# Optimization experiments

Hardware: AMD Instinct MI355X
Metric: run time of the kernel (lower is better)

The kernel has to match this reference:

```python
import jax, jax.numpy as jnp
import numpy as np

V = 4096      # num codes (vocab)
D = 128       # embedding dim
K = 3         # diffusion scales
H = 4         # attn heads
FF = 128      # ff hidden
L = 2         # attn layers
NVIS = 8192   # visits
MAXC = 32     # max codes per visit
PAD = 0


def logmap0(x):
    # Poincare ball (c=1) log map at origin: artanh(||x||) * x / ||x||
    eps = 1e-7
    norm = jnp.linalg.norm(x, axis=-1, keepdims=True)
    norm_c = jnp.clip(norm, eps, 1.0 - 1e-5)
    return jnp.arctanh(norm_c) * x / jnp.maximum(norm, eps)


def layer_norm(x, g, b, eps=1e-5):
    m = jnp.mean(x, axis=-1, keepdims=True)
    v = jnp.mean((x - m) ** 2, axis=-1, keepdims=True)
    return (x - m) * jax.lax.rsqrt(v + eps) * g + b


def attn_block(x, Wqkv, bqkv, Wo, bo, W1, b1, W2, b2, g1, be1, g2, be2):
    # x: [V, D] (batch of 1, squeezed)
    hd = D // H
    qkv = x @ Wqkv.T + bqkv                      # [V, 3D]
    q, k, v = jnp.split(qkv, 3, axis=-1)
    q = q.reshape(V, H, hd)
    k = k.reshape(V, H, hd)
    v = v.reshape(V, H, hd)
    scores = jnp.einsum('shd,thd->hst', q, k) / np.sqrt(hd).astype(x.dtype)
    a = jax.nn.softmax(scores, axis=-1)          # [H, V, V]
    o = jnp.einsum('hst,thd->shd', a, v).reshape(V, D)
    attn_out = o @ Wo.T + bo
    x = layer_norm(x + attn_out, g1, be1)
    ff = jax.nn.gelu(x @ W1.T + b1) @ W2.T + b2
    return layer_norm(x + ff, g2, be2)


def setup_inputs() -> dict:
    key = jax.random.key(0)
    ks = jax.random.split(key, 20)
    inp = {}
    inp['visits'] = jax.random.randint(ks[0], (NVIS, MAXC), 0, V)
    # hyperbolic points inside unit ball
    inp['X_hyp'] = jax.random.normal(ks[1], (V, D), jnp.float32) * 0.01
    inp['kernels'] = jax.random.normal(ks[2], (K, V, V), jnp.float32) / V
    inp['proj_W'] = jax.random.normal(ks[3], (D, K * D), jnp.float32) * 0.05
    inp['proj_b'] = jnp.zeros((D,), jnp.float32)
    s = 0.05
    inp['Wqkv'] = jax.random.normal(ks[4], (L, 3 * D, D), jnp.float32) * s
    inp['bqkv'] = jnp.zeros((L, 3 * D), jnp.float32)
    inp['Wo'] = jax.random.normal(ks[5], (L, D, D), jnp.float32) * s
    inp['bo'] = jnp.zeros((L, D), jnp.float32)
    inp['W1'] = jax.random.normal(ks[6], (L, FF, D), jnp.float32) * s
    inp['b1'] = jnp.zeros((L, FF), jnp.float32)
    inp['W2'] = jax.random.normal(ks[7], (L, D, FF), jnp.float32) * s
    inp['b2'] = jnp.zeros((L, D), jnp.float32)
    inp['ln1_g'] = jnp.ones((L, D), jnp.float32)
    inp['ln1_b'] = jnp.zeros((L, D), jnp.float32)
    inp['ln2_g'] = jnp.ones((L, D), jnp.float32)
    inp['ln2_b'] = jnp.zeros((L, D), jnp.float32)
    return inp


def reference(visits, X_hyp, kernels, proj_W, proj_b, Wqkv, bqkv, Wo, bo,
              W1, b1, W2, b2, ln1_g, ln1_b, ln2_g, ln2_b):
    # ---- hyperbolic graph diffusion ----
    Z0 = logmap0(X_hyp)                              # [V, D]
    Z_scales = jnp.einsum('kuv,vd->ukd', kernels, Z0)  # [V, K, D]
    Z_cat = Z_scales.reshape(V, K * D)
    H_ = Z_cat @ proj_W.T + proj_b                   # [V, D]
    # ---- global self-attention stack ----
    for l in range(L):
        H_ = attn_block(H_, Wqkv[l], bqkv[l], Wo[l], bo[l],
                        W1[l], b1[l], W2[l], b2[l],
                        ln1_g[l], ln1_b[l], ln2_g[l], ln2_b[l])
    # ---- per-visit masked mean pooling (segment mean) ----
    mask = (visits != PAD)                           # [NVIS, MAXC]
    gathered = H_[visits] * mask[..., None]          # [NVIS, MAXC, D]
    cnt = jnp.sum(mask, axis=-1, keepdims=True).astype(H_.dtype)
    summed = jnp.sum(gathered, axis=1)               # [NVIS, D]
    return jnp.where(cnt > 0, summed / jnp.maximum(cnt, 1.0), 0.0)
```

## Files before the change

### kernel.cpp

```cpp
#include <hip/hip_runtime.h>
#include <hip/hip_bf16.h>
#include <math.h>

#define VN 4096
#define DIM 128
#define KS 3
#define NH 4
#define HD 32
#define NVIS 8192
#define MAXC 32
#define KTOT (KS*VN)

typedef unsigned short u16;
typedef __attribute__((ext_vector_type(8))) short short8;
typedef __attribute__((ext_vector_type(4))) float f32x4;
typedef __attribute__((ext_vector_type(4))) float f4v;

__device__ __forceinline__ u16 f2b(float f){
  union { float f; unsigned u; } c; c.f = f;
  unsigned u = c.u;
  return (u16)((u + 0x7fffu + ((u >> 16) & 1u)) >> 16);
}
__device__ __forceinline__ float b2f(u16 x){
  union { float f; unsigned u; } c; c.u = ((unsigned)x) << 16; return c.f;
}
__device__ __forceinline__ unsigned cvt2(float lo, float hi){
  unsigned r;
  asm("v_cvt_pk_bf16_f32 %0, %1, %2" : "=v"(r) : "v"(lo), "v"(hi));
  return r;
}
#define MFMA16(a,b,c) __builtin_amdgcn_mfma_f32_16x16x32_bf16((a),(b),(c),0,0,0)

__global__ __launch_bounds__(256) void k_logmap(const float* __restrict__ xh, u16* __restrict__ z0){
  __shared__ float xs[64][132];
  __shared__ float part[4][64];
  __shared__ float sscale[64];
  int t = threadIdx.x;
  int v0 = blockIdx.x * 64;
  #pragma unroll
  for(int i=0;i<8;i++){
    int id = t + 256*i; int e = id*4; int r = e>>7; int c = e&127;
    float4 u = *(const float4*)&xh[(size_t)(v0+r)*DIM + c];
    xs[r][c+0]=u.x; xs[r][c+1]=u.y; xs[r][c+2]=u.z; xs[r][c+3]=u.w;
  }
  __syncthreads();
  int r = t & 63, q = t >> 6;
  float p = 0.f;
  #pragma unroll
  for(int c=0;c<32;c++){ float x = xs[r][q*32+c]; p += x*x; }
  part[q][r] = p;
  __syncthreads();
  if(t < 64){
    float ss = part[0][t]+part[1][t]+part[2][t]+part[3][t];
    float n = sqrtf(ss);
    float nc = fminf(fmaxf(n, 1e-7f), 1.0f - 1e-5f);
    sscale[t] = atanhf(nc) / fmaxf(n, 1e-7f);
  }
  __syncthreads();
  #pragma unroll
  for(int i=0;i<8;i++){
    int id = t + 256*i; int e = id*4; int rr = e>>7; int cc = e&127;
    float s = sscale[rr];
    uint2 o = { cvt2(xs[rr][cc+0]*s, xs[rr][cc+1]*s),
                cvt2(xs[rr][cc+2]*s, xs[rr][cc+3]*s) };
    *(uint2*)&z0[(size_t)(v0+rr)*DIM + cc] = o;
  }
}

template<bool AF32, bool BF32>
__device__ __forceinline__ void gemm_k128_t(const void* __restrict__ Agv, int lda,
                                            const void* __restrict__ Bgv, int ldb,
                                            u16 (*As)[128*72], u16 (*Bs)[128*72], f32x4 (&acc)[2][8]){
  int t = threadIdx.x;
  int w=t>>6, lane=t&63, l15=lane&15, quad=lane>>4;
  #pragma unroll
  for(int s=0;s<2;s++)
    #pragma unroll
    for(int n=0;n<8;n++) acc[s][n] = (f32x4){0.f,0.f,0.f,0.f};

  float4 af[4][2]; uint4 ai[4];
  float4 bf[4][2]; uint4 bi[4];

  auto LOAD = [&](int kb){
    #pragma unroll
    for(int i=0;i<4;i++){
      int id = t + 256*i; int row = id>>3, c8 = id&7;
      if constexpr(AF32){
        const float* Ag = (const float*)Agv;
        af[i][0] = *(const float4*)&Ag[(size_t)row*lda + kb + c8*8];
        af[i][1] = *(const float4*)&Ag[(size_t)row*lda + kb + c8*8 + 4];
      } else {
        const u16* Ag = (const u16*)Agv;
        ai[i] = *(const uint4*)&Ag[(size_t)row*lda + kb + c8*8];
      }
      if constexpr(BF32){
        const float* Bg = (const float*)Bgv;
        bf[i][0] = *(const float4*)&Bg[(size_t)row*ldb + kb + c8*8];
        bf[i][1] = *(const float4*)&Bg[(size_t)row*ldb + kb + c8*8 + 4];
      } else {
        const u16* Bg = (const u16*)Bgv;
        bi[i] = *(const uint4*)&Bg[(size_t)row*ldb + kb + c8*8];
      }
    }
  };
  auto COMMIT = [&](u16* Ad, u16* Bd){
    #pragma unroll
    for(int i=0;i<4;i++){
      int id = t + 256*i; int row = id>>3, c8 = id&7;
      if constexpr(AF32){
        uint4 p = { cvt2(af[i][0].x, af[i][0].y), cvt2(af[i][0].z, af[i][0].w),
                    cvt2(af[i][1].x, af[i][1].y), cvt2(af[i][1].z, af[i][1].w) };
        *(uint4*)&Ad[row*72 + c8*8] = p;
      } else {
        *(uint4*)&Ad[row*72 + c8*8] = ai[i];
      }
      if constexpr(BF32){
        uint4 q = { cvt2(bf[i][0].x, bf[i][0].y), cvt2(bf[i][0].z, bf[i][0].w),
                    cvt2(bf[i][1].x, bf[i][1].y), cvt2(bf[i][1].z, bf[i][1].w) };
        *(uint4*)&Bd[row*72 + c8*8] = q;
      } else {
        *(uint4*)&Bd[row*72 + c8*8] = bi[i];
      }
    }
  };
  auto COMPUTE = [&](const u16* Asb, const u16* Bsb){
    #pragma unroll
    for(int ks=0; ks<2; ks++){
      short8 a[2], b[8];
      #pragma unroll
      for(int s=0;s<2;s++) a[s] = *(const short8*)&Asb[(w*32+s*16+l15)*72 + (ks*4+quad)*8];
      #pragma unroll
      for(int n=0;n<8;n++)  b[n] = *(const short8*)&Bsb[(n*16+l15)*72 + (ks*4+quad)*8];
      #pragma unroll
      for(int s=0;s<2;s++)
        #pragma unroll
        for(int n=0;n<8;n++) acc[s][n] = MFMA16(a[s], b[n], acc[s][n]);
    }
  };

  LOAD(0);  COMMIT(As[0], Bs[0]);  __syncthreads();
  LOAD(64); COMPUTE(As[0], Bs[0]); COMMIT(As[1], Bs[1]); __syncthreads();
  COMPUTE(As[1], Bs[1]);
}

__global__ __launch_bounds__(256) void k_gproj(const float* __restrict__ projW, const u16* __restrict__ z0,
                                               u16* __restrict__ gbuf){
  __shared__ u16 As[2][128*72], Bs[2][128*72];
  int kb = blockIdx.x >> 5, vt = blockIdx.x & 31;
  f32x4 acc[2][8];
  gemm_k128_t<true,false>(projW + kb*128, 3*DIM, z0 + (size_t)vt*128*DIM, DIM, As, Bs, acc);
  int t=threadIdx.x, w=t>>6, lane=t&63, l15=lane&15, quad=lane>>4;
  #pragma unroll
  for(int s=0;s<2;s++)
    #pragma unroll
    for(int n=0;n<8;n++)
      #pragma unroll
      for(int rg=0;rg<4;rg++){
        int d = w*32 + s*16 + quad*4 + rg;
        int v = vt*128 + n*16 + l15;
        gbuf[(size_t)(d*KS + kb)*VN + v] = f2b(acc[s][n][rg]);
      }
}

__global__ __launch_bounds__(256) void k_diff(const float* __restrict__ kers, const u16* __restrict__ gbuf,
                                              u16* __restrict__ hpart){
  __shared__ u16 As[2][128*72], Bs[2][128*72];
  int t = threadIdx.x;
  int mt = blockIdx.x & 31;
  int sl = blockIdx.x >> 5;
  int w=t>>6, lane=t&63, l15=lane&15, quad=lane>>4;
  f32x4 acc[2][8];
  #pragma unroll
  for(int s=0;s<2;s++)
    #pragma unroll
    for(int n=0;n<8;n++) acc[s][n] = (f32x4){0.f,0.f,0.f,0.f};
  int k0 = sl * 768;

  f4v  fa0[4], fa1[4];
  uint4 fb[4];

  auto LOADSTEP = [&](int step){
    int kk = k0 + step*64;
    int kout = kk >> 12; int vv = kk & 4095;
    #pragma unroll
    for(int i=0;i<4;i++){
      int id = t + 256*i; int row = id>>3, c8 = id&7;
      const float* ap = &kers[((size_t)kout<<24) + (size_t)(mt*128+row)*VN + vv + c8*8];
      fa0[i] = __builtin_nontemporal_load((const f4v*)ap);
      fa1[i] = __builtin_nontemporal_load((const f4v*)(ap+4));
      fb[i]  = *(const uint4*)&gbuf[(size_t)row*KTOT + kk + c8*8];
    }
  };
  auto COMMIT = [&](u16* Ad, u16* Bd){
    #pragma unroll
    for(int i=0;i<4;i++){
      int id = t + 256*i; int row = id>>3, c8 = id&7;
      uint4 pa = { cvt2(fa0[i].x, fa0[i].y), cvt2(fa0[i].z, fa0[i].w),
                   cvt2(fa1[i].x, fa1[i].y), cvt2(fa1[i].z, fa1[i].w) };
      *(uint4*)&Ad[row*72 + c8*8] = pa;
      *(uint4*)&Bd[row*72 + c8*8] = fb[i];
    }
  };
  auto COMPUTE = [&](const u16* Asb, const u16* Bsb){
    #pragma unroll
    for(int ks=0; ks<2; ks++){
      short8 a[2], b[8];
      #pragma unroll
      for(int s=0;s<2;s++) a[s] = *(const short8*)&Asb[(w*32+s*16+l15)*72 + (ks*4+quad)*8];
      #pragma unroll
      for(int n=0;n<8;n++)  b[n] = *(const short8*)&Bsb[(n*16+l15)*72 + (ks*4+quad)*8];
      #pragma unroll
      for(int s=0;s<2;s++)
        #pragma unroll
        for(int n=0;n<8;n++) acc[s][n] = MFMA16(a[s], b[n], acc[s][n]);
    }
  };

  LOADSTEP(0);
  COMMIT(As[0], Bs[0]);
  __syncthreads();
  #pragma unroll 1
  for(int sp=0; sp<6; sp++){
    LOADSTEP(2*sp+1);
    COMPUTE(As[0], Bs[0]);
    COMMIT(As[1], Bs[1]);
    __syncthreads();
    if(sp < 5){
      LOADSTEP(2*sp+2);
      COMPUTE(As[1], Bs[1]);
      COMMIT(As[0], Bs[0]);
      __syncthreads();
    }
  }
  COMPUTE(As[1], Bs[1]);

  u16* dst = hpart + ((size_t)blockIdx.x << 14);
  #pragma unroll
  for(int s=0;s<2;s++)
    #pragma unroll
    for(int n=0;n<8;n++)
      #pragma unroll
      for(int rg=0;rg<4;rg++)
        dst[(w*32+s*16+quad*4+rg)*128 + n*16 + l15] = f2b(acc[s][n][rg]);
}

__global__ __launch_bounds__(256) void k_hreduce(const u16* __restrict__ hpart, const float* __restrict__ pb,
                                                 float* __restrict__ h0){
  int idx = blockIdx.x*256 + threadIdx.x;
  int e0 = idx*4;
  int c0 = e0 & 127;
  float4 r;
  r.x = pb[c0+0]; r.y = pb[c0+1]; r.z = pb[c0+2]; r.w = pb[c0+3];
  #pragma unroll
  for(int sl=0; sl<16; sl++){
    uint2 u = *(const uint2*)&hpart[((size_t)sl<<19) + e0];
    r.x += b2f((u16)(u.x & 0xffffu)); r.y += b2f((u16)(u.x >> 16));
    r.z += b2f((u16)(u.y & 0xffffu)); r.w += b2f((u16)(u.y >> 16));
  }
  *(float4*)&h0[e0] = r;
}

template<bool AF32>
__global__ __launch_bounds__(256) void k_qkv(const void* __restrict__ xb, const float* __restrict__ Wq,
                                             const float* __restrict__ bq, u16* __restrict__ outq){
  __shared__ u16 As[2][128*72], Bs[2][128*72];
  int mt = blockIdx.x & 31, ntile = blockIdx.x >> 5;
  f32x4 acc[2][8];
  const void* Ap = AF32 ? (const void*)((const float*)xb + (size_t)mt*128*DIM)
                        : (const void*)((const u16*)xb + (size_t)mt*128*DIM);
  gemm_k128_t<AF32,true>(Ap, DIM, Wq + (size_t)ntile*128*DIM, DIM, As, Bs, acc);
  int t=threadIdx.x, w=t>>6, lane=t&63, l15=lane&15, quad=lane>>4;
  #pragma unroll
  for(int s=0;s<2;s++)
    #pragma unroll
    for(int n=0;n<8;n++)
      #pragma unroll
      for(int rg=0;rg<4;rg++){
        int row = mt*128 + w*32 + s*16 + quad*4 + rg;
        int col = ntile*128 + n*16 + l15;
        outq[(size_t)row*(3*DIM) + col] = f2b(acc[s][n][rg] + bq[col]);
      }
}

__global__ __launch_bounds__(256) void k_attn(const u16* __restrict__ qkv, float* __restrict__ opart,
                                              float* __restrict__ mlpart){
  __shared__ u16 Qs[64*40];
  __shared__ u16 Ksh[2][128*40];
  __shared__ u16 Vt[2][32*136];
  __shared__ u16 Ps[4*16*136];
  int t=threadIdx.x;
  int b = blockIdx.x;
  int h = b>>7, qt = (b>>1)&63, half = b&1;
  int w=t>>6, lane=t&63, l15=lane&15, quad=lane>>4;
  { int r = t>>2, c = t&3;
    *(uint4*)&Qs[r*40 + c*8] = *(const uint4*)&qkv[(size_t)(qt*64+r)*(3*DIM) + h*HD + c*8];
  }
  int skey = t>>2, sc4 = t&3;
  uint4 kreg[2], vreg[2];
  #pragma unroll
  for(int i=0;i<2;i++){
    int key = skey + 64*i;
    kreg[i] = *(const uint4*)&qkv[(size_t)((size_t)(half*16)*128+key)*(3*DIM) + DIM + h*HD + sc4*8];
    vreg[i] = *(const uint4*)&qkv[(size_t)((size_t)(half*16)*128+key)*(3*DIM) + 2*DIM + h*HD + sc4*8];
  }
  #pragma unroll
  for(int i=0;i<2;i++){
    int key = skey + 64*i;
    *(uint4*)&Ksh[0][key*40 + sc4*8] = kreg[i];
    u16 tmp[8]; *(uint4*)tmp = vreg[i];
    #pragma unroll
    for(int j=0;j<8;j++) Vt[0][(sc4*8+j)*136 + key] = tmp[j];
  }
  __syncthreads();
  short8 aq = *(short8*)&Qs[(w*16+l15)*40 + quad*8];
  f32x4 oacc[2]; oacc[0]=(f32x4){0.f,0.f,0.f,0.f}; oacc[1]=(f32x4){0.f,0.f,0.f,0.f};
  float mrun[4], lrun[4];
  #pragma unroll
  for(int rg=0;rg<4;rg++){ mrun[rg] = -INFINITY; lrun[rg] = 0.f; }
  const float sc = 0.17677669529663687f;
  for(int kti=0;kti<16;kti++){
    int cur = kti&1;
    if(kti<15){
      int kt = half*16 + kti + 1;
      #pragma unroll
      for(int i=0;i<2;i++){
        int key = skey + 64*i;
        kreg[i] = *(const uint4*)&qkv[(size_t)(kt*128+key)*(3*DIM) + DIM + h*HD + sc4*8];
        vreg[i] = *(const uint4*)&qkv[(size_t)(kt*128+key)*(3*DIM) + 2*DIM + h*HD + sc4*8];
      }
    }
    f32x4 s[8];
    #pragma unroll
    for(int n=0;n<8;n++)
      s[n] = MFMA16(aq, *(short8*)&Ksh[cur][(n*16+l15)*40 + quad*8], ((f32x4){0.f,0.f,0.f,0.f}));
    float mx[4];
    #pragma unroll
    for(int rg=0;rg<4;rg++){
      float m = -INFINITY;
      #pragma unroll
      for(int n=0;n<8;n++) m = fmaxf(m, s[n][rg]);
      #pragma unroll
      for(int off=1;off<16;off<<=1) m = fmaxf(m, __shfl_xor(m, off, 64));
      mx[rg] = m;
    }
    float alpha[4], rs[4];
    #pragma unroll
    for(int rg=0;rg<4;rg++){
      float mn = fmaxf(mrun[rg], mx[rg]);
      alpha[rg] = __expf(sc*(mrun[rg] - mn));
      mrun[rg] = mn; rs[rg] = 0.f;
    }
    #pragma unroll
    for(int n=0;n<8;n++)
      #pragma unroll
      for(int rg=0;rg<4;rg++){
        float p = __expf(sc*(s[n][rg] - mrun[rg]));
        s[n][rg] = p; rs[rg] += p;
      }
    #pragma unroll
    for(int rg=0;rg<4;rg++){
      #pragma unroll
      for(int off=1;off<16;off<<=1) rs[rg] += __shfl_xor(rs[rg], off, 64);
      lrun[rg] = lrun[rg]*alpha[rg] + rs[rg];
      oacc[0][rg] *= alpha[rg]; oacc[1][rg] *= alpha[rg];
    }
    #pragma unroll
    for(int n=0;n<8;n++)
      #pragma unroll
      for(int rg=0;rg<4;rg++)
        Ps[w*16*136 + (quad*4+rg)*136 + n*16 + l15] = f2b(s[n][rg]);
    #pragma unroll
    for(int kt2=0;kt2<4;kt2++){
      short8 ap = *(short8*)&Ps[w*16*136 + l15*136 + kt2*32 + quad*8];
      #pragma unroll
      for(int n2=0;n2<2;n2++)
        oacc[n2] = MFMA16(ap, *(short8*)&Vt[cur][(n2*16+l15)*136 + kt2*32 + quad*8], oacc[n2]);
    }
    if(kti<15){
      #pragma unroll
      for(int i=0;i<2;i++){
        int key = skey + 64*i;
        *(uint4*)&Ksh[cur^1][key*40 + sc4*8] = kreg[i];
        u16 tmp[8]; *(uint4*)tmp = vreg[i];
        #pragma unroll
        for(int j=0;j<8;j++) Vt[cur^1][(sc4*8+j)*136 + key] = tmp[j];
      }
    }
    __syncthreads();
  }
  float* op = opart + ((size_t)b << 11);
  #pragma unroll
  for(int n2=0;n2<2;n2++)
    #pragma unroll
    for(int rg=0;rg<4;rg++)
      op[(w*16+quad*4+rg)*32 + n2*16 + l15] = oacc[n2][rg];
  if(l15 == 0){
    float* ml = mlpart + ((size_t)b << 7);
    #pragma unroll
    for(int rg=0;rg<4;rg++){
      int r = w*16 + quad*4 + rg;
      ml[r] = sc*mrun[rg]; ml[64 + r] = lrun[rg];
    }
  }
}

__global__ __launch_bounds__(256) void k_oprojln(const float* __restrict__ opart, const float* __restrict__ mlpart,
                                                 const float* __restrict__ W,
                                                 const float* __restrict__ bias, const float* __restrict__ resf,
                                                 const float* __restrict__ g, const float* __restrict__ bb,
                                                 float* __restrict__ outf, u16* __restrict__ outb){
  __shared__ u16 As[128*72], Bs[128*72];
  int mt = blockIdx.x;
  int t=threadIdx.x, w=t>>6, lane=t&63, l15=lane&15, quad=lane>>4;
  f32x4 acc[2][8];
  #pragma unroll
  for(int s=0;s<2;s++)
    #pragma unroll
    for(int n=0;n<8;n++) acc[s][n] = (f32x4){0.f,0.f,0.f,0.f};
  #pragma unroll
  for(int step=0; step<2; step++){
    int kb = step*64;
    __syncthreads();
    #pragma unroll
    for(int i=0;i<4;i++){
      int id = t + 256*i; int row = id>>3, c8 = id&7;
      int col = kb + c8*8;
      int hh = col>>5, c0 = col&31;
      int grow = mt*128 + row;
      int hq = hh*64 + (grow>>6);
      int rr = grow & 63;
      const float* o0  = opart  + ((size_t)(hq*2)   << 11);
      const float* o1  = opart  + ((size_t)(hq*2+1) << 11);
      const float* ml0 = mlpart + ((size_t)(hq*2)   << 7);
      const float* ml1 = mlpart + ((size_t)(hq*2+1) << 7);
      float m0 = ml0[rr], l0 = ml0[64+rr], m1 = ml1[rr], l1 = ml1[64+rr];
      float m = fmaxf(m0, m1);
      float w0 = __expf(m0 - m), w1 = __expf(m1 - m);
      float inv = 1.f / (l0*w0 + l1*w1);
      float4 a0 = *(const float4*)&o0[rr*32 + c0];
      float4 a1 = *(const float4*)&o0[rr*32 + c0 + 4];
      float4 c0v = *(const float4*)&o1[rr*32 + c0];
      float4 c1v = *(const float4*)&o1[rr*32 + c0 + 4];
      uint4 pa = { cvt2((a0.x*w0+c0v.x*w1)*inv, (a0.y*w0+c0v.y*w1)*inv),
                   cvt2((a0.z*w0+c0v.z*w1)*inv, (a0.w*w0+c0v.w*w1)*inv),
                   cvt2((a1.x*w0+c1v.x*w1)*inv, (a1.y*w0+c1v.y*w1)*inv),
                   cvt2((a1.w*0.f + a1.x*w0 + c1v.x*w1)*inv*0.f + (a1.w*w0+c1v.w*w1)*inv, (a1.w*w0+c1v.w*w1)*inv) };
      pa.w = cvt2((a1.z*w0+c1v.z*w1)*inv, (a1.w*w0+c1v.w*w1)*inv);
      *(uint4*)&As[row*72 + c8*8] = pa;
      float4 f0 = *(const float4*)&W[(size_t)row*DIM + kb + c8*8];
      float4 f1 = *(const float4*)&W[(size_t)row*DIM + kb + c8*8 + 4];
      uint4 qa = { cvt2(f0.x, f0.y), cvt2(f0.z, f0.w),
                   cvt2(f1.x, f1.y), cvt2(f1.z, f1.w) };
      *(uint4*)&Bs[row*72 + c8*8] = qa;
    }
    __syncthreads();
    #pragma unroll
    for(int ks=0; ks<2; ks++){
      short8 a[2], b[8];
      #pragma unroll
      for(int s=0;s<2;s++) a[s] = *(short8*)&As[(w*32+s*16+l15)*72 + (ks*4+quad)*8];
      #pragma unroll
      for(int n=0;n<8;n++)  b[n] = *(short8*)&Bs[(n*16+l15)*72 + (ks*4+quad)*8];
      #pragma unroll
      for(int s=0;s<2;s++)
        #pragma unroll
        for(int n=0;n<8;n++) acc[s][n] = MFMA16(a[s], b[n], acc[s][n]);
    }
  }
  #pragma unroll
  for(int s=0;s<2;s++)
    #pragma unroll
    for(int n=0;n<8;n++)
      #pragma unroll
      for(int rg=0;rg<4;rg++){
        int row = mt*128 + w*32 + s*16 + quad*4 + rg;
        int col = n*16 + l15;
        acc[s][n][rg] += bias[col] + resf[(size_t)row*DIM + col];
      }
  #pragma unroll
  for(int s=0;s<2;s++)
    #pragma unroll
    for(int rg=0;rg<4;rg++){
      float a=0.f, bsum=0.f;
      #pragma unroll
      for(int n=0;n<8;n++){ float x = acc[s][n][rg]; a += x; bsum += x*x; }
      #pragma unroll
      for(int off=1;off<16;off<<=1){ a += __shfl_xor(a, off, 64); bsum += __shfl_xor(bsum, off, 64); }
      float mean = a*(1.f/128.f);
      float var  = bsum*(1.f/128.f) - mean*mean;
      float rstd = rsqrtf(var + 1e-5f);
      #pragma unroll
      for(int n=0;n<8;n++){
        int row = mt*128 + w*32 + s*16 + quad*4 + rg;
        int col = n*16 + l15;
        float y = (acc[s][n][rg] - mean)*rstd*g[col] + bb[col];
        outf[(size_t)row*DIM + col] = y;
        outb[(size_t)row*DIM + col] = f2b(y);
      }
    }
}

__global__ __launch_bounds__(256) void k_projln(const u16* __restrict__ Ab, const float* __restrict__ W,
                                                const float* __restrict__ bias, const float* __restrict__ resf,
                                                const float* __restrict__ g, const float* __restrict__ bb,
                                                float* __restrict__ outf, u16* __restrict__ outb){
  __shared__ u16 As[2][128*72], Bs[2][128*72];
  int mt = blockIdx.x;
  f32x4 acc[2][8];
  gemm_k128_t<false,true>(Ab + (size_t)mt*128*DIM, DIM, W, DIM, As, Bs, acc);
  int t=threadIdx.x, w=t>>6, lane=t&63, l15=lane&15, quad=lane>>4;
  #pragma unroll
  for(int s=0;s<2;s++)
    #pragma unroll
    for(int n=0;n<8;n++)
      #pragma unroll
      for(int rg=0;rg<4;rg++){
        int row = mt*128 + w*32 + s*16 + quad*4 + rg;
        int col = n*16 + l15;
        acc[s][n][rg] += bias[col] + resf[(size_t)row*DIM + col];
      }
  #pragma unroll
  for(int s=0;s<2;s++)
    #pragma unroll
    for(int rg=0;rg<4;rg++){
      float a=0.f, bsum=0.f;
      #pragma unroll
      for(int n=0;n<8;n++){ float x = acc[s][n][rg]; a += x; bsum += x*x; }
      #pragma unroll
      for(int off=1;off<16;off<<=1){ a += __shfl_xor(a, off, 64); bsum += __shfl_xor(bsum, off, 64); }
      float mean = a*(1.f/128.f);
      float var  = bsum*(1.f/128.f) - mean*mean;
      float rstd = rsqrtf(var + 1e-5f);
      #pragma unroll
      for(int n=0;n<8;n++){
        int row = mt*128 + w*32 + s*16 + quad*4 + rg;
        int col = n*16 + l15;
        float y = (acc[s][n][rg] - mean)*rstd*g[col] + bb[col];
        outf[(size_t)row*DIM + col] = y;
        outb[(size_t)row*DIM + col] = f2b(y);
      }
    }
}

__global__ __launch_bounds__(256) void k_ff1(const u16* __restrict__ Ab, const float* __restrict__ W,
                                             const float* __restrict__ bias, u16* __restrict__ outb){
  __shared__ u16 As[2][128*72], Bs[2][128*72];
  int mt = blockIdx.x;
  f32x4 acc[2][8];
  gemm_k128_t<false,true>(Ab + (size_t)mt*128*DIM, DIM, W, DIM, As, Bs, acc);
  int t=threadIdx.x, w=t>>6, lane=t&63, l15=lane&15, quad=lane>>4;
  #pragma unroll
  for(int s=0;s<2;s++)
    #pragma unroll
    for(int n=0;n<8;n++)
      #pragma unroll
      for(int rg=0;rg<4;rg++){
        int row = mt*128 + w*32 + s*16 + quad*4 + rg;
        int col = n*16 + l15;
        float v = acc[s][n][rg] + bias[col];
        float z = 0.7978845608028654f*(v + 0.044715f*v*v*v);
        float e = __expf(2.f*z);
        float th = 1.f - 2.f/(e + 1.f);
        outb[(size_t)row*DIM + col] = f2b(0.5f*v*(1.f + th));
      }
}

__global__ __launch_bounds__(256) void k_pool(const int* __restrict__ visits, const float* __restrict__ xf,
                                              float* __restrict__ out){
  int t = threadIdx.x;
  int vis = blockIdx.x*2 + (t>>7);
  int col = t & 127;
  float s = 0.f; int cnt = 0;
  #pragma unroll
  for(int j=0;j<MAXC;j++){
    int idx = visits[vis*MAXC + j];
    if(idx != 0){ s += xf[(size_t)idx*DIM + col]; cnt++; }
  }
  float r = (cnt > 0) ? s/(float)cnt : 0.f;
  out[(size_t)vis*DIM + col] = r;
}

extern "C" void kernel_launch(void* const* d_in, const int* in_sizes, int n_in,
                              void* d_out, int out_size, void* d_ws, size_t ws_size,
                              hipStream_t stream){
  (void)in_sizes; (void)n_in; (void)out_size; (void)ws_size;
  const int*   visits = (const int*)d_in[0];
  const float* xhyp  = (const float*)d_in[1];
  const float* kers  = (const float*)d_in[2];
  const float* projW = (const float*)d_in[3];
  const float* projb = (const float*)d_in[4];
  const float* Wqkv  = (const float*)d_in[5];
  const float* bqkv  = (const float*)d_in[6];
  const float* Wo    = (const float*)d_in[7];
  const float* bo    = (const float*)d_in[8];
  const float* W1    = (const float*)d_in[9];
  const float* b1    = (const float*)d_in[10];
  const float* W2    = (const float*)d_in[11];
  const float* b2    = (const float*)d_in[12];
  const float* g1    = (const float*)d_in[13];
  const float* be1   = (const float*)d_in[14];
  const float* g2    = (const float*)d_in[15];
  const float* be2   = (const float*)d_in[16];

  char* ws = (char*)d_ws;
  u16*   z0    = (u16*)(ws);
  u16*   gbuf  = (u16*)(ws + (1u<<20));
  float* h0    = (float*)(ws + (4u<<20));
  u16*   qkvb  = (u16*)(ws + (7u<<20));
  float* ln1f  = (float*)(ws + (11u<<20));
  u16*   ln1b  = (u16*)(ws + (13u<<20));
  u16*   ffa   = (u16*)(ws + (14u<<20));
  float* x1f   = (float*)(ws + (15u<<20));
  u16*   x1b   = (u16*)(ws + (17u<<20));
  float* x2f   = (float*)(ws + (18u<<20));
  u16*   x2b   = (u16*)(ws + (20u<<20));
  u16*   hpart = (u16*)(ws + (21u<<20));
  float* opart = (float*)(ws + (53u<<20));
  float* mlprt = (float*)(ws + (57u<<20));

  k_logmap<<<64,256,0,stream>>>(xhyp, z0);
  k_gproj<<<96,256,0,stream>>>(projW, z0, gbuf);
  k_diff<<<512,256,0,stream>>>(kers, gbuf, hpart);
  k_hreduce<<<512,256,0,stream>>>(hpart, projb, h0);

  const void* curA = (const void*)h0; bool af32 = true;
  const float* curf = h0;
  float* outfs[2] = {x1f, x2f}; u16* outbs[2] = {x1b, x2b};
  for(int l=0;l<2;l++){
    if(af32) k_qkv<true ><<<96,256,0,stream>>>(curA, Wqkv + (size_t)l*3*DIM*DIM, bqkv + (size_t)l*3*DIM, qkvb);
    else     k_qkv<false><<<96,256,0,stream>>>(curA, Wqkv + (size_t)l*3*DIM*DIM, bqkv + (size_t)l*3*DIM, qkvb);
    k_attn<<<512,256,0,stream>>>(qkvb, opart, mlprt);
    k_oprojln<<<32,256,0,stream>>>(opart, mlprt, Wo + (size_t)l*DIM*DIM, bo + (size_t)l*DIM, curf,
                                   g1 + (size_t)l*DIM, be1 + (size_t)l*DIM, ln1f, ln1b);
    k_ff1<<<32,256,0,stream>>>(ln1b, W1 + (size_t)l*DIM*DIM, b1 + (size_t)l*DIM, ffa);
    k_projln<<<32,256,0,stream>>>(ffa, W2 + (size_t)l*DIM*DIM, b2 + (size_t)l*DIM, ln1f,
                                  g2 + (size_t)l*DIM, be2 + (size_t)l*DIM, outfs[l], outbs[l]);
    curA = (const void*)outbs[l]; af32 = false; curf = outfs[l];
  }
  k_pool<<<4096,256,0,stream>>>(visits, curf, (float*)d_out);
}
```

Measured before the change: 555.4 us.

## Fuse out-proj, LN, FFN, LN and next-layer QKV into one kernel; lazy softmax rescale

Replaces the separate out-projection+LN, FF1 and FF2+LN kernels, plus the second layer's QKV projection, with one per-row-tile kernel. Intermediates stay in LDS and registers instead of going through global memory, which cuts several launches and round trips. The attention loop now rescales the running max, sum and output only when some lane's max grows, skipping exp and multiply work on most key tiles. The fused kernel runs on only 32 blocks and does more serial work per block, including three extra QKV GEMM passes, so it may leave the GPU underused.

```diff
diff --git a/kernel.cpp b/kernel.cpp
--- a/kernel.cpp
+++ b/kernel.cpp
@@ -343,13 +343,22 @@
       for(int off=1;off<16;off<<=1) m = fmaxf(m, __shfl_xor(m, off, 64));
       mx[rg] = m;
     }
-    float alpha[4], rs[4];
-    #pragma unroll
-    for(int rg=0;rg<4;rg++){
-      float mn = fmaxf(mrun[rg], mx[rg]);
-      alpha[rg] = __expf(sc*(mrun[rg] - mn));
-      mrun[rg] = mn; rs[rg] = 0.f;
-    }
+    bool grew = false;
+    #pragma unroll
+    for(int rg=0;rg<4;rg++) grew = grew || (mx[rg] > mrun[rg]);
+    if(__any(grew)){
+      #pragma unroll
+      for(int rg=0;rg<4;rg++){
+        float mn = fmaxf(mrun[rg], mx[rg]);
+        float alpha = __expf(sc*(mrun[rg] - mn));
+        mrun[rg] = mn;
+        lrun[rg] *= alpha;
+        oacc[0][rg] *= alpha; oacc[1][rg] *= alpha;
+      }
+    }
+    float rs[4];
+    #pragma unroll
+    for(int rg=0;rg<4;rg++) rs[rg] = 0.f;
     #pragma unroll
     for(int n=0;n<8;n++)
       #pragma unroll
@@ -361,8 +370,7 @@
     for(int rg=0;rg<4;rg++){
       #pragma unroll
       for(int off=1;off<16;off<<=1) rs[rg] += __shfl_xor(rs[rg], off, 64);
-      lrun[rg] = lrun[rg]*alpha[rg] + rs[rg];
-      oacc[0][rg] *= alpha[rg]; oacc[1][rg] *= alpha[rg];
+      lrun[rg] += rs[rg];
     }
     #pragma unroll
     for(int n=0;n<8;n++)
@@ -404,23 +412,89 @@
   }
 }
 
-__global__ __launch_bounds__(256) void k_oprojln(const float* __restrict__ opart, const float* __restrict__ mlpart,
-                                                 const float* __restrict__ W,
-                                                 const float* __restrict__ bias, const float* __restrict__ resf,
-                                                 const float* __restrict__ g, const float* __restrict__ bb,
-                                                 float* __restrict__ outf, u16* __restrict__ outb){
-  __shared__ u16 As[128*72], Bs[128*72];
+template<bool QKV>
+__global__ __launch_bounds__(256) void k_fused(const float* __restrict__ opart, const float* __restrict__ mlpart,
+                                               const float* __restrict__ Wo, const float* __restrict__ bo,
+                                               const float* __restrict__ resf,
+                                               const float* __restrict__ g1, const float* __restrict__ be1,
+                                               const float* __restrict__ W1, const float* __restrict__ b1,
+                                               const float* __restrict__ W2, const float* __restrict__ b2,
+                                               const float* __restrict__ g2, const float* __restrict__ be2,
+                                               float* __restrict__ outf,
+                                               const float* __restrict__ Wq, const float* __restrict__ bq,
+                                               u16* __restrict__ qkvout){
+  __shared__ u16 As[2][128*72], Bs[2][128*72];
   int mt = blockIdx.x;
   int t=threadIdx.x, w=t>>6, lane=t&63, l15=lane&15, quad=lane>>4;
-  f32x4 acc[2][8];
-  #pragma unroll
-  for(int s=0;s<2;s++)
-    #pragma unroll
-    for(int n=0;n<8;n++) acc[s][n] = (f32x4){0.f,0.f,0.f,0.f};
+  f32x4 acc[2][8], y1[2][8];
+
+  auto ZERO = [&](){
+    #pragma unroll
+    for(int s=0;s<2;s++)
+      #pragma unroll
+      for(int n=0;n<8;n++) acc[s][n] = (f32x4){0.f,0.f,0.f,0.f};
+  };
+  auto COMPUTE = [&](const u16* Asb, const u16* Bsb){
+    #pragma unroll
+    for(int ks=0; ks<2; ks++){
+      short8 a[2], b[8];
+      #pragma unroll
+      for(int s=0;s<2;s++) a[s] = *(const short8*)&Asb[(w*32+s*16+l15)*72 + (ks*4+quad)*8];
+      #pragma unroll
+      for(int n=0;n<8;n++)  b[n] = *(const short8*)&Bsb[(n*16+l15)*72 + (ks*4+quad)*8];
+      #pragma unroll
+      for(int s=0;s<2;s++)
+        #pragma unroll
+        for(int n=0;n<8;n++) acc[s][n] = MFMA16(a[s], b[n], acc[s][n]);
+    }
+  };
+  auto STAGE_W = [&](const float* __restrict__ Wp){
+    #pragma unroll
+    for(int step=0;step<2;step++)
+      #pragma unroll
+      for(int i=0;i<4;i++){
+        int id = t + 256*i; int row = id>>3, c8 = id&7;
+        float4 f0 = *(const float4*)&Wp[(size_t)row*DIM + step*64 + c8*8];
+        float4 f1 = *(const float4*)&Wp[(size_t)row*DIM + step*64 + c8*8 + 4];
+        uint4 q = { cvt2(f0.x,f0.y), cvt2(f0.z,f0.w), cvt2(f1.x,f1.y), cvt2(f1.z,f1.w) };
+        *(uint4*)&Bs[step][row*72 + c8*8] = q;
+      }
+  };
+  auto WRITE_A = [&](f32x4 (&y)[2][8]){
+    #pragma unroll
+    for(int s=0;s<2;s++)
+      #pragma unroll
+      for(int n=0;n<8;n++)
+        #pragma unroll
+        for(int rg=0;rg<4;rg++){
+          int r = w*32 + s*16 + quad*4 + rg;
+          As[n>>2][r*72 + (n&3)*16 + l15] = f2b(y[s][n][rg]);
+        }
+  };
+  auto LNROW = [&](const float* __restrict__ g, const float* __restrict__ bv){
+    #pragma unroll
+    for(int s=0;s<2;s++)
+      #pragma unroll
+      for(int rg=0;rg<4;rg++){
+        float a=0.f, bs=0.f;
+        #pragma unroll
+        for(int n=0;n<8;n++){ float x = acc[s][n][rg]; a += x; bs += x*x; }
+        #pragma unroll
+        for(int off=1;off<16;off<<=1){ a += __shfl_xor(a, off, 64); bs += __shfl_xor(bs, off, 64); }
+        float mean = a*(1.f/128.f);
+        float var  = bs*(1.f/128.f) - mean*mean;
+        float rstd = rsqrtf(var + 1e-5f);
+        #pragma unroll
+        for(int n=0;n<8;n++){
+          int col = n*16 + l15;
+          acc[s][n][rg] = (acc[s][n][rg] - mean)*rstd*g[col] + bv[col];
+        }
+      }
+  };
+
   #pragma unroll
   for(int step=0; step<2; step++){
     int kb = step*64;
-    __syncthreads();
     #pragma unroll
     for(int i=0;i<4;i++){
       int id = t + 256*i; int row = id>>3, c8 = id&7;
@@ -437,36 +511,24 @@
       float m = fmaxf(m0, m1);
       float w0 = __expf(m0 - m), w1 = __expf(m1 - m);
       float inv = 1.f / (l0*w0 + l1*w1);
-      float4 a0 = *(const float4*)&o0[rr*32 + c0];
-      float4 a1 = *(const float4*)&o0[rr*32 + c0 + 4];
+      float4 a0  = *(const float4*)&o0[rr*32 + c0];
+      float4 a1  = *(const float4*)&o0[rr*32 + c0 + 4];
       float4 c0v = *(const float4*)&o1[rr*32 + c0];
       float4 c1v = *(const float4*)&o1[rr*32 + c0 + 4];
-      uint4 pa = { cvt2((a0.x*w0+c0v.x*w1)*inv, (a0.y*w0+c0v.y*w1)*inv),
-                   cvt2((a0.z*w0+c0v.z*w1)*inv, (a0.w*w0+c0v.w*w1)*inv),
-                   cvt2((a1.x*w0+c1v.x*w1)*inv, (a1.y*w0+c1v.y*w1)*inv),
-                   cvt2((a1.w*0.f + a1.x*w0 + c1v.x*w1)*inv*0.f + (a1.w*w0+c1v.w*w1)*inv, (a1.w*w0+c1v.w*w1)*inv) };
+      uint4 pa;
+      pa.x = cvt2((a0.x*w0+c0v.x*w1)*inv, (a0.y*w0+c0v.y*w1)*inv);
+      pa.y = cvt2((a0.z*w0+c0v.z*w1)*inv, (a0.w*w0+c0v.w*w1)*inv);
+      pa.z = cvt2((a1.x*w0+c1v.x*w1)*inv, (a1.y*w0+c1v.y*w1)*inv);
       pa.w = cvt2((a1.z*w0+c1v.z*w1)*inv, (a1.w*w0+c1v.w*w1)*inv);
-      *(uint4*)&As[row*72 + c8*8] = pa;
-      float4 f0 = *(const float4*)&W[(size_t)row*DIM + kb + c8*8];
-      float4 f1 = *(const float4*)&W[(size_t)row*DIM + kb + c8*8 + 4];
-      uint4 qa = { cvt2(f0.x, f0.y), cvt2(f0.z, f0.w),
-                   cvt2(f1.x, f1.y), cvt2(f1.z, f1.w) };
-      *(uint4*)&Bs[row*72 + c8*8] = qa;
-    }
-    __syncthreads();
-    #pragma unroll
-    for(int ks=0; ks<2; ks++){
-      short8 a[2], b[8];
-      #pragma unroll
-      for(int s=0;s<2;s++) a[s] = *(short8*)&As[(w*32+s*16+l15)*72 + (ks*4+quad)*8];
-      #pragma unroll
-      for(int n=0;n<8;n++)  b[n] = *(short8*)&Bs[(n*16+l15)*72 + (ks*4+quad)*8];
-      #pragma unroll
-      for(int s=0;s<2;s++)
-        #pragma unroll
-        for(int n=0;n<8;n++) acc[s][n] = MFMA16(a[s], b[n], acc[s][n]);
-    }
-  }
+      *(uint4*)&As[step][row*72 + c8*8] = pa;
+      float4 f0 = *(const float4*)&Wo[(size_t)row*DIM + kb + c8*8];
+      float4 f1 = *(const float4*)&Wo[(size_t)row*DIM + kb + c8*8 + 4];
+      uint4 qa = { cvt2(f0.x,f0.y), cvt2(f0.z,f0.w), cvt2(f1.x,f1.y), cvt2(f1.z,f1.w) };
+      *(uint4*)&Bs[step][row*72 + c8*8] = qa;
+    }
+  }
+  __syncthreads();
+  ZERO(); COMPUTE(As[0], Bs[0]); COMPUTE(As[1], Bs[1]);
   #pragma unroll
   for(int s=0;s<2;s++)
     #pragma unroll
@@ -475,94 +537,75 @@
       for(int rg=0;rg<4;rg++){
         int row = mt*128 + w*32 + s*16 + quad*4 + rg;
         int col = n*16 + l15;
-        acc[s][n][rg] += bias[col] + resf[(size_t)row*DIM + col];
-      }
-  #pragma unroll
-  for(int s=0;s<2;s++)
-    #pragma unroll
-    for(int rg=0;rg<4;rg++){
-      float a=0.f, bsum=0.f;
-      #pragma unroll
-      for(int n=0;n<8;n++){ float x = acc[s][n][rg]; a += x; bsum += x*x; }
-      #pragma unroll
-      for(int off=1;off<16;off<<=1){ a += __shfl_xor(a, off, 64); bsum += __shfl_xor(bsum, off, 64); }
-      float mean = a*(1.f/128.f);
-      float var  = bsum*(1.f/128.f) - mean*mean;
-      float rstd = rsqrtf(var + 1e-5f);
-      #pragma unroll
-      for(int n=0;n<8;n++){
-        int row = mt*128 + w*32 + s*16 + quad*4 + rg;
+        acc[s][n][rg] += bo[col] + resf[(size_t)row*DIM + col];
+      }
+  LNROW(g1, be1);
+  #pragma unroll
+  for(int s=0;s<2;s++)
+    #pragma unroll
+    for(int n=0;n<8;n++) y1[s][n] = acc[s][n];
+  __syncthreads();
+  WRITE_A(y1); STAGE_W(W1);
+  __syncthreads();
+  ZERO(); COMPUTE(As[0], Bs[0]); COMPUTE(As[1], Bs[1]);
+  #pragma unroll
+  for(int s=0;s<2;s++)
+    #pragma unroll
+    for(int n=0;n<8;n++)
+      #pragma unroll
+      for(int rg=0;rg<4;rg++){
         int col = n*16 + l15;
-        float y = (acc[s][n][rg] - mean)*rstd*g[col] + bb[col];
-        outf[(size_t)row*DIM + col] = y;
-        outb[(size_t)row*DIM + col] = f2b(y);
-      }
-    }
-}
-
-__global__ __launch_bounds__(256) void k_projln(const u16* __restrict__ Ab, const float* __restrict__ W,
-                                                const float* __restrict__ bias, const float* __restrict__ resf,
-                                                const float* __restrict__ g, const float* __restrict__ bb,
-                                                float* __restrict__ outf, u16* __restrict__ outb){
-  __shared__ u16 As[2][128*72], Bs[2][128*72];
-  int mt = blockIdx.x;
-  f32x4 acc[2][8];
-  gemm_k128_t<false,true>(Ab + (size_t)mt*128*DIM, DIM, W, DIM, As, Bs, acc);
-  int t=threadIdx.x, w=t>>6, lane=t&63, l15=lane&15, quad=lane>>4;
-  #pragma unroll
-  for(int s=0;s<2;s++)
-    #pragma unroll
-    for(int n=0;n<8;n++)
-      #pragma unroll
-      for(int rg=0;rg<4;rg++){
-        int row = mt*128 + w*32 + s*16 + quad*4 + rg;
-        int col = n*16 + l15;
-        acc[s][n][rg] += bias[col] + resf[(size_t)row*DIM + col];
-      }
-  #pragma unroll
-  for(int s=0;s<2;s++)
-    #pragma unroll
-    for(int rg=0;rg<4;rg++){
-      float a=0.f, bsum=0.f;
-      #pragma unroll
-      for(int n=0;n<8;n++){ float x = acc[s][n][rg]; a += x; bsum += x*x; }
-      #pragma unroll
-      for(int off=1;off<16;off<<=1){ a += __shfl_xor(a, off, 64); bsum += __shfl_xor(bsum, off, 64); }
-      float mean = a*(1.f/128.f);
-      float var  = bsum*(1.f/128.f) - mean*mean;
-      float rstd = rsqrtf(var + 1e-5f);
-      #pragma unroll
-      for(int n=0;n<8;n++){
-        int row = mt*128 + w*32 + s*16 + quad*4 + rg;
-        int col = n*16 + l15;
-        float y = (acc[s][n][rg] - mean)*rstd*g[col] + bb[col];
-        outf[(size_t)row*DIM + col] = y;
-        outb[(size_t)row*DIM + col] = f2b(y);
-      }
-    }
-}
-
-__global__ __launch_bounds__(256) void k_ff1(const u16* __restrict__ Ab, const float* __restrict__ W,
-                                             const float* __restrict__ bias, u16* __restrict__ outb){
-  __shared__ u16 As[2][128*72], Bs[2][128*72];
-  int mt = blockIdx.x;
-  f32x4 acc[2][8];
-  gemm_k128_t<false,true>(Ab + (size_t)mt*128*DIM, DIM, W, DIM, As, Bs, acc);
-  int t=threadIdx.x, w=t>>6, lane=t&63, l15=lane&15, quad=lane>>4;
-  #pragma unroll
-  for(int s=0;s<2;s++)
-    #pragma unroll
-    for(int n=0;n<8;n++)
-      #pragma unroll
-      for(int rg=0;rg<4;rg++){
-        int row = mt*128 + w*32 + s*16 + quad*4 + rg;
-        int col = n*16 + l15;
-        float v = acc[s][n][rg] + bias[col];
+        float v = acc[s][n][rg] + b1[col];
         float z = 0.7978845608028654f*(v + 0.044715f*v*v*v);
         float e = __expf(2.f*z);
         float th = 1.f - 2.f/(e + 1.f);
-        outb[(size_t)row*DIM + col] = f2b(0.5f*v*(1.f + th));
-      }
+        acc[s][n][rg] = 0.5f*v*(1.f + th);
+      }
+  __syncthreads();
+  WRITE_A(acc); STAGE_W(W2);
+  __syncthreads();
+  ZERO(); COMPUTE(As[0], Bs[0]); COMPUTE(As[1], Bs[1]);
+  #pragma unroll
+  for(int s=0;s<2;s++)
+    #pragma unroll
+    for(int n=0;n<8;n++)
+      #pragma unroll
+      for(int rg=0;rg<4;rg++){
+        int col = n*16 + l15;
+        acc[s][n][rg] += b2[col] + y1[s][n][rg];
+      }
+  LNROW(g2, be2);
+  #pragma unroll
+  for(int s=0;s<2;s++)
+    #pragma unroll
+    for(int n=0;n<8;n++)
+      #pragma unroll
+      for(int rg=0;rg<4;rg++){
+        int row = mt*128 + w*32 + s*16 + quad*4 + rg;
+        int col = n*16 + l15;
+        outf[(size_t)row*DIM + col] = acc[s][n][rg];
+      }
+  if constexpr(QKV){
+    __syncthreads();
+    WRITE_A(acc);
+    #pragma unroll 1
+    for(int nt=0; nt<3; nt++){
+      STAGE_W(Wq + (size_t)nt*DIM*DIM);
+      __syncthreads();
+      ZERO(); COMPUTE(As[0], Bs[0]); COMPUTE(As[1], Bs[1]);
+      #pragma unroll
+      for(int s=0;s<2;s++)
+        #pragma unroll
+        for(int n=0;n<8;n++)
+          #pragma unroll
+          for(int rg=0;rg<4;rg++){
+            int row = mt*128 + w*32 + s*16 + quad*4 + rg;
+            int col = nt*128 + n*16 + l15;
+            qkvout[(size_t)row*(3*DIM) + col] = f2b(acc[s][n][rg] + bq[col]);
+          }
+      __syncthreads();
+    }
+  }
 }
 
 __global__ __launch_bounds__(256) void k_pool(const int* __restrict__ visits, const float* __restrict__ xf,
@@ -607,13 +650,8 @@
   u16*   gbuf  = (u16*)(ws + (1u<<20));
   float* h0    = (float*)(ws + (4u<<20));
   u16*   qkvb  = (u16*)(ws + (7u<<20));
-  float* ln1f  = (float*)(ws + (11u<<20));
-  u16*   ln1b  = (u16*)(ws + (13u<<20));
-  u16*   ffa   = (u16*)(ws + (14u<<20));
   float* x1f   = (float*)(ws + (15u<<20));
-  u16*   x1b   = (u16*)(ws + (17u<<20));
   float* x2f   = (float*)(ws + (18u<<20));
-  u16*   x2b   = (u16*)(ws + (20u<<20));
   u16*   hpart = (u16*)(ws + (21u<<20));
   float* opart = (float*)(ws + (53u<<20));
   float* mlprt = (float*)(ws + (57u<<20));
@@ -623,19 +661,15 @@
   k_diff<<<512,256,0,stream>>>(kers, gbuf, hpart);
   k_hreduce<<<512,256,0,stream>>>(hpart, projb, h0);
 
-  const void* curA = (const void*)h0; bool af32 = true;
-  const float* curf = h0;
-  float* outfs[2] = {x1f, x2f}; u16* outbs[2] = {x1b, x2b};
-  for(int l=0;l<2;l++){
-    if(af32) k_qkv<true ><<<96,256,0,stream>>>(curA, Wqkv + (size_t)l*3*DIM*DIM, bqkv + (size_t)l*3*DIM, qkvb);
-    else     k_qkv<false><<<96,256,0,stream>>>(curA, Wqkv + (size_t)l*3*DIM*DIM, bqkv + (size_t)l*3*DIM, qkvb);
-    k_attn<<<512,256,0,stream>>>(qkvb, opart, mlprt);
-    k_oprojln<<<32,256,0,stream>>>(opart, mlprt, Wo + (size_t)l*DIM*DIM, bo + (size_t)l*DIM, curf,
-                                   g1 + (size_t)l*DIM, be1 + (size_t)l*DIM, ln1f, ln1b);
-    k_ff1<<<32,256,0,stream>>>(ln1b, W1 + (size_t)l*DIM*DIM, b1 + (size_t)l*DIM, ffa);
-    k_projln<<<32,256,0,stream>>>(ffa, W2 + (size_t)l*DIM*DIM, b2 + (size_t)l*DIM, ln1f,
-                                  g2 + (size_t)l*DIM, be2 + (size_t)l*DIM, outfs[l], outbs[l]);
-    curA = (const void*)outbs[l]; af32 = false; curf = outfs[l];
-  }
-  k_pool<<<4096,256,0,stream>>>(visits, curf, (float*)d_out);
-}
+  k_qkv<true><<<96,256,0,stream>>>((const void*)h0, Wqkv, bqkv, qkvb);
+  k_attn<<<512,256,0,stream>>>(qkvb, opart, mlprt);
+  k_fused<true><<<32,256,0,stream>>>(opart, mlprt, Wo, bo, h0, g1, be1,
+                                     W1, b1, W2, b2, g2, be2, x1f,
+                                     Wqkv + (size_t)3*DIM*DIM, bqkv + 3*DIM, qkvb);
+  k_attn<<<512,256,0,stream>>>(qkvb, opart, mlprt);
+  k_fused<false><<<32,256,0,stream>>>(opart, mlprt, Wo + (size_t)DIM*DIM, bo + DIM, x1f,
+                                      g1 + DIM, be1 + DIM, W1 + (size_t)DIM*DIM, b1 + DIM,
+                                      W2 + (size_t)DIM*DIM, b2 + DIM, g2 + DIM, be2 + DIM, x2f,
+                                      nullptr, nullptr, nullptr);
+  k_pool<<<4096,256,0,stream>>>(visits, x2f, (float*)d_out);
+}
```

Measured after the change: 793.9 us. 1.43x slower.
